# Kernel tuning notes

Hardware: AMD Instinct MI355X
Metric: run time of the kernel (lower is better)

## Reference

```python
import jax, jax.numpy as jnp
import numpy as np

B, D, H = 262144, 8, 64  # batch, in_out_dim, hidden_dim


def _lin_init(k, fan_in, fan_out):
    k1, k2 = jax.random.split(k)
    s = 1.0 / np.sqrt(fan_in)
    W = jax.random.uniform(k1, (fan_in, fan_out), minval=-s, maxval=s, dtype=jnp.float32)
    b = jax.random.uniform(k2, (fan_out,), minval=-s, maxval=s, dtype=jnp.float32)
    return W, b


def setup_inputs():
    key = jax.random.key(0)
    ks = jax.random.split(key, 12)
    w1_0, b1_0 = _lin_init(ks[0], D + 1, H)
    w1_1, b1_1 = _lin_init(ks[1], H, H)
    w1_2, b1_2 = _lin_init(ks[2], H, H)
    w1_o, b1_o = _lin_init(ks[3], H, D)
    w2_0, b2_0 = _lin_init(ks[4], D + 1, H)
    w2_1, b2_1 = _lin_init(ks[5], H, H)
    w2_2, b2_2 = _lin_init(ks[6], H, H)
    w2_o, b2_o = _lin_init(ks[7], H, 1)
    t = jax.random.uniform(ks[8], (), dtype=jnp.float32)
    z = jax.random.normal(ks[9], (B, D), dtype=jnp.float32)
    logp_z = jnp.zeros((B, 1), dtype=jnp.float32)
    return dict(t=t, z=z, logp_z=logp_z,
                w1_0=w1_0, b1_0=b1_0, w1_1=w1_1, b1_1=b1_1, w1_2=w1_2, b1_2=b1_2,
                w1_o=w1_o, b1_o=b1_o,
                w2_0=w2_0, b2_0=b2_0, w2_1=w2_1, b2_1=b2_1, w2_2=w2_2, b2_2=b2_2,
                w2_o=w2_o, b2_o=b2_o)


def reference(t, z, logp_z,
              w1_0, b1_0, w1_1, b1_1, w1_2, b1_2, w1_o, b1_o,
              w2_0, b2_0, w2_1, b2_1, w2_2, b2_2, w2_o, b2_o):
    Bz, Dz = z.shape
    tcol = jnp.full((Bz, 1), t, dtype=z.dtype)  # t repeated per-sample, detached constant

    def net1(zz):  # HyperNetwork1: dz/dt field, Tanh MLP, (B,D+1)->(B,D)
        s = jnp.concatenate([tcol, zz], axis=1)
        x = jnp.tanh(s @ w1_0 + b1_0)
        x = jnp.tanh(x @ w1_1 + b1_1)
        x = jnp.tanh(x @ w1_2 + b1_2)
        return x @ w1_o + b1_o

    dz_dt = net1(z)

    # HyperNetwork2: growth term g, (B,D+1)->(B,1)
    s = jnp.concatenate([tcol, z], axis=1)
    x = jnp.tanh(s @ w2_0 + b2_0)
    x = jnp.tanh(x @ w2_1 + b2_1)
    x = jnp.tanh(x @ w2_2 + b2_2)
    g = x @ w2_o + b2_o

    # Exact trace of d(dz_dt)/dz via D forward-mode JVPs (vectorized, replaces
    # the per-dim autograd.grad loop in trace_df_dz).
    eye = jnp.eye(Dz, dtype=z.dtype)
    jv = jax.vmap(lambda e: jax.jvp(net1, (z,), (jnp.broadcast_to(e, z.shape),))[1])(eye)  # (D,B,D)
    trace = jnp.diagonal(jv, axis1=0, axis2=2).sum(-1)  # (B,)

    dlogp_z_dt = g - trace[:, None]
    return (dz_dt, dlogp_z_dt, g)
```

## Files before the change

### kernel.cpp

```cpp
#include <hip/hip_runtime.h>


#define BATCH 262144

typedef _Float16 h16;
typedef __attribute__((ext_vector_type(8))) _Float16 half8;
typedef __attribute__((ext_vector_type(4))) float f32x4;

#define MFMA16(a, b, c) __builtin_amdgcn_mfma_f32_16x16x32_f16((a), (b), (c), 0, 0, 0)

#define WS_A   0
#define WS_WO  61440
#define WS_E   62464
#define WS_B   64512
#define WS_BO  66048

__device__ __forceinline__ float tanh_fast(float x) {
    float e = __builtin_amdgcn_exp2f(x * 2.8853900817779268f);
    return 1.0f - 2.0f * __builtin_amdgcn_rcpf(e + 1.0f);
}

__global__ void __launch_bounds__(256) prep(
    const float* __restrict__ w1_0, const float* __restrict__ w1_1,
    const float* __restrict__ w1_2, const float* __restrict__ w1_o,
    const float* __restrict__ w2_0, const float* __restrict__ w2_1,
    const float* __restrict__ w2_2, const float* __restrict__ w2_o,
    const float* __restrict__ b1_0, const float* __restrict__ b1_1,
    const float* __restrict__ b1_2, const float* __restrict__ b1_o,
    const float* __restrict__ b2_0, const float* __restrict__ b2_1,
    const float* __restrict__ b2_2, char* __restrict__ ws)
{
    int t = blockIdx.x * 256 + threadIdx.x;
    if (t < 3840) {
        int slot = t >> 6, lane = t & 63;
        int mrow = lane & 15, kg = lane >> 4;
        half8 v;
        #pragma unroll
        for (int kk = 0; kk < 8; ++kk) {
            int mt = 0, ks = 0;
            float val = 0.0f;
            if (slot < 4) {
                mt = slot; int k = kg * 8 + kk; int m = mt * 16 + mrow;
                val = (k < 9) ? w1_0[k * 64 + m] : 0.0f;
            } else if (slot < 12) {
                int s = slot - 4; mt = s >> 1; ks = s & 1;
                int k = ks * 32 + kg * 8 + kk; int m = mt * 16 + mrow;
                val = w1_1[k * 64 + m];
            } else if (slot < 20) {
                int s = slot - 12; mt = s >> 1; ks = s & 1;
                int k = ks * 32 + kg * 8 + kk; int m = mt * 16 + mrow;
                val = w1_2[k * 64 + m];
            } else if (slot < 22) {
                ks = slot - 20; int k = ks * 32 + kg * 8 + kk;
                val = (mrow < 8) ? w1_o[k * 8 + mrow] : 0.0f;
            } else if (slot < 26) {
                mt = slot - 22; int k = kg * 8 + kk; int m = mt * 16 + mrow;
                val = (k < 9) ? w2_0[k * 64 + m] : 0.0f;
            } else if (slot < 34) {
                int s = slot - 26; mt = s >> 1; ks = s & 1;
                int k = ks * 32 + kg * 8 + kk; int m = mt * 16 + mrow;
                val = w2_1[k * 64 + m];
            } else if (slot < 42) {
                int s = slot - 34; mt = s >> 1; ks = s & 1;
                int k = ks * 32 + kg * 8 + kk; int m = mt * 16 + mrow;
                val = w2_2[k * 64 + m];
            } else if (slot < 44) {
                ks = slot - 42; int k = ks * 32 + kg * 8 + kk;
                val = (mrow == 0) ? w2_o[k] : 0.0f;
            } else if (slot < 52) {
                int s = slot - 44; mt = s >> 1; ks = s & 1;
                int k = ks * 32 + kg * 8 + kk; int m = mt * 16 + mrow;
                val = w1_2[m * 64 + k];
            } else {
                int s = slot - 52; mt = s >> 1; ks = s & 1;
                int k = ks * 32 + kg * 8 + kk; int m = mt * 16 + mrow;
                val = w1_1[m * 64 + k];
            }
            v[kk] = (h16)val;
        }
        *(half8*)((h16*)(ws + WS_A) + (size_t)slot * 512 + (size_t)lane * 8) = v;
    } else if (t < 4352) {
        int e = t - 3840; int d = e >> 6, k = e & 63;
        ((h16*)(ws + WS_WO))[e] = (h16)w1_o[k * 8 + d];
    } else if (t < 4864) {
        int e = t - 4352; int d = e >> 6, g = (e >> 4) & 3, tr = e & 15;
        int mt = tr >> 2, r = tr & 3;
        int k = 16 * mt + 4 * g + r;
        ((float*)(ws + WS_E))[e] = w1_0[(d + 1) * 64 + k];
    } else if (t < 5248) {
        int e = t - 4864; int layer = e >> 6, i = e & 63;
        int g = i >> 4, mt = (i >> 2) & 3, r = i & 3;
        int m = 16 * mt + 4 * g + r;
        const float* bsrc = (layer == 0) ? b1_0 : (layer == 1) ? b1_1 :
                            (layer == 2) ? b1_2 : (layer == 3) ? b2_0 :
                            (layer == 4) ? b2_1 : b2_2;
        ((float*)(ws + WS_B))[e] = bsrc[m];
    } else if (t < 5264) {
        int i = t - 5248; int g = i >> 2, r = i & 3;
        int m = 4 * g + r;
        ((float*)(ws + WS_BO))[i] = (m < 8) ? b1_o[m] : 0.0f;
    }
}

__global__ void __launch_bounds__(256) cnf_mfma(
    const float* __restrict__ tp, const float* __restrict__ zp,
    const float* __restrict__ b2_o, const char* __restrict__ ws,
    float* __restrict__ out)
{
    __shared__ __align__(16) h16 xbuf[4][1024];
    __shared__ __align__(16) h16 t3buf[4][1024];

    const int lane = threadIdx.x & 63;
    const int wv = threadIdx.x >> 6;
    const int c = lane & 15;
    const int g = lane >> 4;
    const int sIdx = blockIdx.x * 64 + wv * 16 + c;
    const int swz = (c & 7) << 3;

    const h16*   wsA  = (const h16*)(ws + WS_A);
    const h16*   wsWo = (const h16*)(ws + WS_WO);
    const float* wsE  = (const float*)(ws + WS_E);
    const float* wsB  = (const float*)(ws + WS_B);
    const float* wsBo = (const float*)(ws + WS_BO);
    h16* xb  = xbuf[wv];
    h16* t3b = t3buf[wv];

    const float tt = tp[0];
    const f32x4 zl = *(const f32x4*)(zp + (size_t)sIdx * 8);
    const f32x4 zh = *(const f32x4*)(zp + (size_t)sIdx * 8 + 4);

    half8 b0f;
    #pragma unroll
    for (int i = 0; i < 8; ++i) b0f[i] = (h16)0.0f;
    if (g == 0) {
        b0f[0] = (h16)tt;
        b0f[1] = (h16)zl[0]; b0f[2] = (h16)zl[1]; b0f[3] = (h16)zl[2];
        b0f[4] = (h16)zl[3]; b0f[5] = (h16)zh[0]; b0f[6] = (h16)zh[1];
        b0f[7] = (h16)zh[2];
    } else if (g == 1) {
        b0f[0] = (h16)zh[3];
    }

    f32x4 d[4], t1v[4], t2v[4];

    #pragma unroll
    for (int mt = 0; mt < 4; ++mt) {
        f32x4 acc = *(const f32x4*)(wsB + 0 * 64 + g * 16 + mt * 4);
        d[mt] = MFMA16(*(const half8*)(wsA + (0 + mt) * 512 + lane * 8), b0f, acc);
    }
    #pragma unroll
    for (int mt = 0; mt < 4; ++mt) {
        union { h16 h[4]; uint2 u; } px;
        #pragma unroll
        for (int r = 0; r < 4; ++r) {
            float x = tanh_fast(d[mt][r]);
            t1v[mt][r] = fmaf(-x, x, 1.0f);
            px.h[r] = (h16)x;
        }
        *(uint2*)&xb[(c * 64 + mt * 16 + 4 * g) ^ swz] = px.u;
    }

    {
        half8 bf0 = *(const half8*)&xb[(c * 64 + 8 * g) ^ swz];
        half8 bf1 = *(const half8*)&xb[(c * 64 + 32 + 8 * g) ^ swz];
        #pragma unroll
        for (int mt = 0; mt < 4; ++mt) {
            f32x4 acc = *(const f32x4*)(wsB + 1 * 64 + g * 16 + mt * 4);
            acc = MFMA16(*(const half8*)(wsA + (4 + mt * 2) * 512 + lane * 8), bf0, acc);
            acc = MFMA16(*(const half8*)(wsA + (5 + mt * 2) * 512 + lane * 8), bf1, acc);
            d[mt] = acc;
        }
    }
    #pragma unroll
    for (int mt = 0; mt < 4; ++mt) {
        union { h16 h[4]; uint2 u; } px;
        #pragma unroll
        for (int r = 0; r < 4; ++r) {
            float x = tanh_fast(d[mt][r]);
            t2v[mt][r] = fmaf(-x, x, 1.0f);
            px.h[r] = (h16)x;
        }
        *(uint2*)&xb[(c * 64 + mt * 16 + 4 * g) ^ swz] = px.u;
    }

    {
        half8 bf0 = *(const half8*)&xb[(c * 64 + 8 * g) ^ swz];
        half8 bf1 = *(const half8*)&xb[(c * 64 + 32 + 8 * g) ^ swz];
        #pragma unroll
        for (int mt = 0; mt < 4; ++mt) {
            f32x4 acc = *(const f32x4*)(wsB + 2 * 64 + g * 16 + mt * 4);
            acc = MFMA16(*(const half8*)(wsA + (12 + mt * 2) * 512 + lane * 8), bf0, acc);
            acc = MFMA16(*(const half8*)(wsA + (13 + mt * 2) * 512 + lane * 8), bf1, acc);
            d[mt] = acc;
        }
    }
    #pragma unroll
    for (int mt = 0; mt < 4; ++mt) {
        union { h16 h[4]; uint2 u; } px, pt;
        #pragma unroll
        for (int r = 0; r < 4; ++r) {
            float x = tanh_fast(d[mt][r]);
            float tq = fmaf(-x, x, 1.0f);
            px.h[r] = (h16)x;
            pt.h[r] = (h16)tq;
        }
        int e = (c * 64 + mt * 16 + 4 * g) ^ swz;
        *(uint2*)&xb[e] = px.u;
        *(uint2*)&t3b[e] = pt.u;
    }

    {
        half8 bf0 = *(const half8*)&xb[(c * 64 + 8 * g) ^ swz];
        half8 bf1 = *(const half8*)&xb[(c * 64 + 32 + 8 * g) ^ swz];
        f32x4 dz = *(const f32x4*)(wsBo + g * 4);
        dz = MFMA16(*(const half8*)(wsA + 20 * 512 + lane * 8), bf0, dz);
        dz = MFMA16(*(const half8*)(wsA + 21 * 512 + lane * 8), bf1, dz);
        if (g < 2)
            *(f32x4*)(out + (size_t)sIdx * 8 + g * 4) = dz;
    }

    #pragma unroll
    for (int mt = 0; mt < 4; ++mt) {
        f32x4 acc = *(const f32x4*)(wsB + 3 * 64 + g * 16 + mt * 4);
        d[mt] = MFMA16(*(const half8*)(wsA + (22 + mt) * 512 + lane * 8), b0f, acc);
    }
    #pragma unroll
    for (int mt = 0; mt < 4; ++mt) {
        union { h16 h[4]; uint2 u; } px;
        #pragma unroll
        for (int r = 0; r < 4; ++r) px.h[r] = (h16)tanh_fast(d[mt][r]);
        *(uint2*)&xb[(c * 64 + mt * 16 + 4 * g) ^ swz] = px.u;
    }
    #pragma unroll 1
    for (int L = 0; L < 2; ++L) {
        int sbase = (L == 0) ? 26 : 34;
        half8 bf0 = *(const half8*)&xb[(c * 64 + 8 * g) ^ swz];
        half8 bf1 = *(const half8*)&xb[(c * 64 + 32 + 8 * g) ^ swz];
        #pragma unroll
        for (int mt = 0; mt < 4; ++mt) {
            f32x4 acc = *(const f32x4*)(wsB + (4 + L) * 64 + g * 16 + mt * 4);
            acc = MFMA16(*(const half8*)(wsA + (sbase + mt * 2) * 512 + lane * 8), bf0, acc);
            acc = MFMA16(*(const half8*)(wsA + (sbase + mt * 2 + 1) * 512 + lane * 8), bf1, acc);
            d[mt] = acc;
        }
        #pragma unroll
        for (int mt = 0; mt < 4; ++mt) {
            union { h16 h[4]; uint2 u; } px;
            #pragma unroll
            for (int r = 0; r < 4; ++r) px.h[r] = (h16)tanh_fast(d[mt][r]);
            *(uint2*)&xb[(c * 64 + mt * 16 + 4 * g) ^ swz] = px.u;
        }
    }
    float gval;
    {
        half8 bf0 = *(const half8*)&xb[(c * 64 + 8 * g) ^ swz];
        half8 bf1 = *(const half8*)&xb[(c * 64 + 32 + 8 * g) ^ swz];
        float b2 = b2_o[0];
        f32x4 acc = {b2, 0.0f, 0.0f, 0.0f};
        acc = MFMA16(*(const half8*)(wsA + 42 * 512 + lane * 8), bf0, acc);
        acc = MFMA16(*(const half8*)(wsA + 43 * 512 + lane * 8), bf1, acc);
        gval = acc[0];
    }

    float tr = 0.0f;
    #pragma unroll 1
    for (int d0 = 0; d0 < 8; ++d0) {
        f32x4 e0 = *(const f32x4*)(wsE + d0 * 64 + g * 16 + 0);
        f32x4 e1 = *(const f32x4*)(wsE + d0 * 64 + g * 16 + 4);
        f32x4 e2 = *(const f32x4*)(wsE + d0 * 64 + g * 16 + 8);
        f32x4 e3 = *(const f32x4*)(wsE + d0 * 64 + g * 16 + 12);
        half8 w0f = *(const half8*)(wsWo + d0 * 64 + 8 * g);
        half8 w1f = *(const half8*)(wsWo + d0 * 64 + 32 + 8 * g);
        half8 t3f0 = *(const half8*)&t3b[(c * 64 + 8 * g) ^ swz];
        half8 t3f1 = *(const half8*)&t3b[(c * 64 + 32 + 8 * g) ^ swz];
        half8 sA0 = t3f0 * w0f;
        half8 sA1 = t3f1 * w1f;
        f32x4 rr[4];
        #pragma unroll
        for (int mt = 0; mt < 4; ++mt) {
            f32x4 acc = {0.0f, 0.0f, 0.0f, 0.0f};
            acc = MFMA16(*(const half8*)(wsA + (44 + mt * 2) * 512 + lane * 8), sA0, acc);
            acc = MFMA16(*(const half8*)(wsA + (45 + mt * 2) * 512 + lane * 8), sA1, acc);
            rr[mt] = acc;
        }
        #pragma unroll
        for (int mt = 0; mt < 4; ++mt) {
            union { h16 h[4]; uint2 u; } px;
            #pragma unroll
            for (int r = 0; r < 4; ++r)
                px.h[r] = (h16)(t2v[mt][r] * rr[mt][r]);
            *(uint2*)&xb[(c * 64 + mt * 16 + 4 * g) ^ swz] = px.u;
        }
        half8 sb0 = *(const half8*)&xb[(c * 64 + 8 * g) ^ swz];
        half8 sb1 = *(const half8*)&xb[(c * 64 + 32 + 8 * g) ^ swz];
        #pragma unroll
        for (int mt = 0; mt < 4; ++mt) {
            f32x4 acc = {0.0f, 0.0f, 0.0f, 0.0f};
            acc = MFMA16(*(const half8*)(wsA + (52 + mt * 2) * 512 + lane * 8), sb0, acc);
            acc = MFMA16(*(const half8*)(wsA + (53 + mt * 2) * 512 + lane * 8), sb1, acc);
            d[mt] = acc;
        }
        #pragma unroll
        for (int r = 0; r < 4; ++r) {
            tr = fmaf(d[0][r] * t1v[0][r], e0[r], tr);
            tr = fmaf(d[1][r] * t1v[1][r], e1[r], tr);
            tr = fmaf(d[2][r] * t1v[2][r], e2[r], tr);
            tr = fmaf(d[3][r] * t1v[3][r], e3[r], tr);
        }
    }
    tr += __shfl_xor(tr, 16);
    tr += __shfl_xor(tr, 32);

    if (g == 0) {
        out[(size_t)BATCH * 8 + sIdx] = gval - tr;
        out[(size_t)BATCH * 9 + sIdx] = gval;
    }
}

extern "C" void kernel_launch(void* const* d_in, const int* in_sizes, int n_in,
                              void* d_out, int out_size, void* d_ws, size_t ws_size,
                              hipStream_t stream) {
    const float* tp   = (const float*)d_in[0];
    const float* zp   = (const float*)d_in[1];
    const float* w1_0 = (const float*)d_in[3];
    const float* b1_0 = (const float*)d_in[4];
    const float* w1_1 = (const float*)d_in[5];
    const float* b1_1 = (const float*)d_in[6];
    const float* w1_2 = (const float*)d_in[7];
    const float* b1_2 = (const float*)d_in[8];
    const float* w1_o = (const float*)d_in[9];
    const float* b1_o = (const float*)d_in[10];
    const float* w2_0 = (const float*)d_in[11];
    const float* b2_0 = (const float*)d_in[12];
    const float* w2_1 = (const float*)d_in[13];
    const float* b2_1 = (const float*)d_in[14];
    const float* w2_2 = (const float*)d_in[15];
    const float* b2_2 = (const float*)d_in[16];
    const float* w2_o = (const float*)d_in[17];
    const float* b2_o = (const float*)d_in[18];

    char* ws = (char*)d_ws;
    float* out = (float*)d_out;

    hipLaunchKernelGGL(prep, dim3(21), dim3(256), 0, stream,
                       w1_0, w1_1, w1_2, w1_o, w2_0, w2_1, w2_2, w2_o,
                       b1_0, b1_1, b1_2, b1_o, b2_0, b2_1, b2_2, ws);
    hipLaunchKernelGGL(cnf_mfma, dim3(BATCH / 64), dim3(256), 0, stream,
                       tp, zp, b2_o, ws, out);
}
```

Before: 186.3 us.

## Reorder trace loop before net2, drop t3 LDS buffer, pack fp16 conversions

```diff
diff --git a/kernel.cpp b/kernel.cpp
--- a/kernel.cpp
+++ b/kernel.cpp
@@ -4,6 +4,7 @@
 #define BATCH 262144
 
 typedef _Float16 h16;
+typedef __attribute__((ext_vector_type(2))) __fp16 f16x2;
 typedef __attribute__((ext_vector_type(8))) _Float16 half8;
 typedef __attribute__((ext_vector_type(4))) float f32x4;
 
@@ -108,7 +109,6 @@
     float* __restrict__ out)
 {
     __shared__ __align__(16) h16 xbuf[4][1024];
-    __shared__ __align__(16) h16 t3buf[4][1024];
 
     const int lane = threadIdx.x & 63;
     const int wv = threadIdx.x >> 6;
@@ -116,14 +116,19 @@
     const int g = lane >> 4;
     const int sIdx = blockIdx.x * 64 + wv * 16 + c;
     const int swz = (c & 7) << 3;
+    h16* xb = xbuf[wv];
+
+    int wadr[4];
+    #pragma unroll
+    for (int mt = 0; mt < 4; ++mt) wadr[mt] = (c * 64 + mt * 16 + 4 * g) ^ swz;
+    const int radr0 = (c * 64 + 8 * g) ^ swz;
+    const int radr1 = (c * 64 + 32 + 8 * g) ^ swz;
 
     const h16*   wsA  = (const h16*)(ws + WS_A);
     const h16*   wsWo = (const h16*)(ws + WS_WO);
     const float* wsE  = (const float*)(ws + WS_E);
     const float* wsB  = (const float*)(ws + WS_B);
     const float* wsBo = (const float*)(ws + WS_BO);
-    h16* xb  = xbuf[wv];
-    h16* t3b = t3buf[wv];
 
     const float tt = tp[0];
     const f32x4 zl = *(const f32x4*)(zp + (size_t)sIdx * 8);
@@ -141,7 +146,8 @@
         b0f[0] = (h16)zh[3];
     }
 
-    f32x4 d[4], t1v[4], t2v[4];
+    f32x4 d[4], t1v[4];
+    f16x2 t2h[8];
 
     #pragma unroll
     for (int mt = 0; mt < 4; ++mt) {
@@ -150,19 +156,19 @@
     }
     #pragma unroll
     for (int mt = 0; mt < 4; ++mt) {
-        union { h16 h[4]; uint2 u; } px;
-        #pragma unroll
-        for (int r = 0; r < 4; ++r) {
-            float x = tanh_fast(d[mt][r]);
-            t1v[mt][r] = fmaf(-x, x, 1.0f);
-            px.h[r] = (h16)x;
-        }
-        *(uint2*)&xb[(c * 64 + mt * 16 + 4 * g) ^ swz] = px.u;
-    }
-
-    {
-        half8 bf0 = *(const half8*)&xb[(c * 64 + 8 * g) ^ swz];
-        half8 bf1 = *(const half8*)&xb[(c * 64 + 32 + 8 * g) ^ swz];
+        float x0 = tanh_fast(d[mt][0]), x1 = tanh_fast(d[mt][1]);
+        float x2 = tanh_fast(d[mt][2]), x3 = tanh_fast(d[mt][3]);
+        t1v[mt][0] = fmaf(-x0, x0, 1.0f); t1v[mt][1] = fmaf(-x1, x1, 1.0f);
+        t1v[mt][2] = fmaf(-x2, x2, 1.0f); t1v[mt][3] = fmaf(-x3, x3, 1.0f);
+        union { f16x2 h[2]; uint2 u; } pk;
+        pk.h[0] = __builtin_amdgcn_cvt_pkrtz(x0, x1);
+        pk.h[1] = __builtin_amdgcn_cvt_pkrtz(x2, x3);
+        *(uint2*)&xb[wadr[mt]] = pk.u;
+    }
+
+    {
+        half8 bf0 = *(const half8*)&xb[radr0];
+        half8 bf1 = *(const half8*)&xb[radr1];
         #pragma unroll
         for (int mt = 0; mt < 4; ++mt) {
             f32x4 acc = *(const f32x4*)(wsB + 1 * 64 + g * 16 + mt * 4);
@@ -173,19 +179,19 @@
     }
     #pragma unroll
     for (int mt = 0; mt < 4; ++mt) {
-        union { h16 h[4]; uint2 u; } px;
-        #pragma unroll
-        for (int r = 0; r < 4; ++r) {
-            float x = tanh_fast(d[mt][r]);
-            t2v[mt][r] = fmaf(-x, x, 1.0f);
-            px.h[r] = (h16)x;
-        }
-        *(uint2*)&xb[(c * 64 + mt * 16 + 4 * g) ^ swz] = px.u;
-    }
-
-    {
-        half8 bf0 = *(const half8*)&xb[(c * 64 + 8 * g) ^ swz];
-        half8 bf1 = *(const half8*)&xb[(c * 64 + 32 + 8 * g) ^ swz];
+        float x0 = tanh_fast(d[mt][0]), x1 = tanh_fast(d[mt][1]);
+        float x2 = tanh_fast(d[mt][2]), x3 = tanh_fast(d[mt][3]);
+        t2h[2 * mt]     = __builtin_amdgcn_cvt_pkrtz(fmaf(-x0, x0, 1.0f), fmaf(-x1, x1, 1.0f));
+        t2h[2 * mt + 1] = __builtin_amdgcn_cvt_pkrtz(fmaf(-x2, x2, 1.0f), fmaf(-x3, x3, 1.0f));
+        union { f16x2 h[2]; uint2 u; } pk;
+        pk.h[0] = __builtin_amdgcn_cvt_pkrtz(x0, x1);
+        pk.h[1] = __builtin_amdgcn_cvt_pkrtz(x2, x3);
+        *(uint2*)&xb[wadr[mt]] = pk.u;
+    }
+
+    {
+        half8 bf0 = *(const half8*)&xb[radr0];
+        half8 bf1 = *(const half8*)&xb[radr1];
         #pragma unroll
         for (int mt = 0; mt < 4; ++mt) {
             f32x4 acc = *(const f32x4*)(wsB + 2 * 64 + g * 16 + mt * 4);
@@ -196,29 +202,86 @@
     }
     #pragma unroll
     for (int mt = 0; mt < 4; ++mt) {
-        union { h16 h[4]; uint2 u; } px, pt;
-        #pragma unroll
-        for (int r = 0; r < 4; ++r) {
-            float x = tanh_fast(d[mt][r]);
-            float tq = fmaf(-x, x, 1.0f);
-            px.h[r] = (h16)x;
-            pt.h[r] = (h16)tq;
-        }
-        int e = (c * 64 + mt * 16 + 4 * g) ^ swz;
-        *(uint2*)&xb[e] = px.u;
-        *(uint2*)&t3b[e] = pt.u;
-    }
-
-    {
-        half8 bf0 = *(const half8*)&xb[(c * 64 + 8 * g) ^ swz];
-        half8 bf1 = *(const half8*)&xb[(c * 64 + 32 + 8 * g) ^ swz];
+        float x0 = tanh_fast(d[mt][0]), x1 = tanh_fast(d[mt][1]);
+        float x2 = tanh_fast(d[mt][2]), x3 = tanh_fast(d[mt][3]);
+        union { f16x2 h[2]; uint2 u; } pk;
+        pk.h[0] = __builtin_amdgcn_cvt_pkrtz(x0, x1);
+        pk.h[1] = __builtin_amdgcn_cvt_pkrtz(x2, x3);
+        *(uint2*)&xb[wadr[mt]] = pk.u;
+    }
+
+    half8 gA[8];
+    #pragma unroll
+    for (int s = 0; s < 8; ++s)
+        gA[s] = *(const half8*)(wsA + (44 + s) * 512 + lane * 8);
+
+    half8 xf0 = *(const half8*)&xb[radr0];
+    half8 xf1 = *(const half8*)&xb[radr1];
+
+    {
         f32x4 dz = *(const f32x4*)(wsBo + g * 4);
-        dz = MFMA16(*(const half8*)(wsA + 20 * 512 + lane * 8), bf0, dz);
-        dz = MFMA16(*(const half8*)(wsA + 21 * 512 + lane * 8), bf1, dz);
+        dz = MFMA16(*(const half8*)(wsA + 20 * 512 + lane * 8), xf0, dz);
+        dz = MFMA16(*(const half8*)(wsA + 21 * 512 + lane * 8), xf1, dz);
         if (g < 2)
             *(f32x4*)(out + (size_t)sIdx * 8 + g * 4) = dz;
     }
 
+    half8 one8;
+    #pragma unroll
+    for (int i = 0; i < 8; ++i) one8[i] = (h16)1.0f;
+    const half8 t3f0 = one8 - xf0 * xf0;
+    const half8 t3f1 = one8 - xf1 * xf1;
+
+    f32x4 tacc[4];
+    #pragma unroll
+    for (int mt = 0; mt < 4; ++mt) tacc[mt] = (f32x4){0.0f, 0.0f, 0.0f, 0.0f};
+
+    #pragma unroll 1
+    for (int d0 = 0; d0 < 8; ++d0) {
+        half8 w0f = *(const half8*)(wsWo + d0 * 64 + 8 * g);
+        half8 w1f = *(const half8*)(wsWo + d0 * 64 + 32 + 8 * g);
+        half8 sA0 = t3f0 * w0f;
+        half8 sA1 = t3f1 * w1f;
+        f32x4 rr[4];
+        #pragma unroll
+        for (int mt = 0; mt < 4; ++mt) {
+            f32x4 acc = {0.0f, 0.0f, 0.0f, 0.0f};
+            acc = MFMA16(gA[2 * mt], sA0, acc);
+            acc = MFMA16(gA[2 * mt + 1], sA1, acc);
+            rr[mt] = acc;
+        }
+        #pragma unroll
+        for (int mt = 0; mt < 4; ++mt) {
+            union { f16x2 h[2]; uint2 u; } pk;
+            pk.h[0] = __builtin_amdgcn_cvt_pkrtz(rr[mt][0], rr[mt][1]) * t2h[2 * mt];
+            pk.h[1] = __builtin_amdgcn_cvt_pkrtz(rr[mt][2], rr[mt][3]) * t2h[2 * mt + 1];
+            *(uint2*)&xb[wadr[mt]] = pk.u;
+        }
+        half8 sb0 = *(const half8*)&xb[radr0];
+        half8 sb1 = *(const half8*)&xb[radr1];
+        #pragma unroll
+        for (int mt = 0; mt < 4; ++mt) {
+            f32x4 acc = {0.0f, 0.0f, 0.0f, 0.0f};
+            acc = MFMA16(*(const half8*)(wsA + (52 + mt * 2) * 512 + lane * 8), sb0, acc);
+            acc = MFMA16(*(const half8*)(wsA + (53 + mt * 2) * 512 + lane * 8), sb1, acc);
+            f32x4 e = *(const f32x4*)(wsE + d0 * 64 + g * 16 + mt * 4);
+            #pragma unroll
+            for (int r = 0; r < 4; ++r) tacc[mt][r] = fmaf(acc[r], e[r], tacc[mt][r]);
+        }
+    }
+    float tr;
+    {
+        f32x4 tm = tacc[0] * t1v[0];
+        #pragma unroll
+        for (int mt = 1; mt < 4; ++mt) {
+            #pragma unroll
+            for (int r = 0; r < 4; ++r) tm[r] = fmaf(tacc[mt][r], t1v[mt][r], tm[r]);
+        }
+        tr = tm[0] + tm[1] + tm[2] + tm[3];
+    }
+    tr += __shfl_xor(tr, 16);
+    tr += __shfl_xor(tr, 32);
+
     #pragma unroll
     for (int mt = 0; mt < 4; ++mt) {
         f32x4 acc = *(const f32x4*)(wsB + 3 * 64 + g * 16 + mt * 4);
@@ -226,16 +289,16 @@
     }
     #pragma unroll
     for (int mt = 0; mt < 4; ++mt) {
-        union { h16 h[4]; uint2 u; } px;
-        #pragma unroll
-        for (int r = 0; r < 4; ++r) px.h[r] = (h16)tanh_fast(d[mt][r]);
-        *(uint2*)&xb[(c * 64 + mt * 16 + 4 * g) ^ swz] = px.u;
+        union { f16x2 h[2]; uint2 u; } pk;
+        pk.h[0] = __builtin_amdgcn_cvt_pkrtz(tanh_fast(d[mt][0]), tanh_fast(d[mt][1]));
+        pk.h[1] = __builtin_amdgcn_cvt_pkrtz(tanh_fast(d[mt][2]), tanh_fast(d[mt][3]));
+        *(uint2*)&xb[wadr[mt]] = pk.u;
     }
     #pragma unroll 1
     for (int L = 0; L < 2; ++L) {
         int sbase = (L == 0) ? 26 : 34;
-        half8 bf0 = *(const half8*)&xb[(c * 64 + 8 * g) ^ swz];
-        half8 bf1 = *(const half8*)&xb[(c * 64 + 32 + 8 * g) ^ swz];
+        half8 bf0 = *(const half8*)&xb[radr0];
+        half8 bf1 = *(const half8*)&xb[radr1];
         #pragma unroll
         for (int mt = 0; mt < 4; ++mt) {
             f32x4 acc = *(const f32x4*)(wsB + (4 + L) * 64 + g * 16 + mt * 4);
@@ -245,71 +308,21 @@
         }
         #pragma unroll
         for (int mt = 0; mt < 4; ++mt) {
-            union { h16 h[4]; uint2 u; } px;
-            #pragma unroll
-            for (int r = 0; r < 4; ++r) px.h[r] = (h16)tanh_fast(d[mt][r]);
-            *(uint2*)&xb[(c * 64 + mt * 16 + 4 * g) ^ swz] = px.u;
+            union { f16x2 h[2]; uint2 u; } pk;
+            pk.h[0] = __builtin_amdgcn_cvt_pkrtz(tanh_fast(d[mt][0]), tanh_fast(d[mt][1]));
+            pk.h[1] = __builtin_amdgcn_cvt_pkrtz(tanh_fast(d[mt][2]), tanh_fast(d[mt][3]));
+            *(uint2*)&xb[wadr[mt]] = pk.u;
         }
     }
     float gval;
     {
-        half8 bf0 = *(const half8*)&xb[(c * 64 + 8 * g) ^ swz];
-        half8 bf1 = *(const half8*)&xb[(c * 64 + 32 + 8 * g) ^ swz];
-        float b2 = b2_o[0];
-        f32x4 acc = {b2, 0.0f, 0.0f, 0.0f};
+        half8 bf0 = *(const half8*)&xb[radr0];
+        half8 bf1 = *(const half8*)&xb[radr1];
+        f32x4 acc = {b2_o[0], 0.0f, 0.0f, 0.0f};
         acc = MFMA16(*(const half8*)(wsA + 42 * 512 + lane * 8), bf0, acc);
         acc = MFMA16(*(const half8*)(wsA + 43 * 512 + lane * 8), bf1, acc);
         gval = acc[0];
     }
-
-    float tr = 0.0f;
-    #pragma unroll 1
-    for (int d0 = 0; d0 < 8; ++d0) {
-        f32x4 e0 = *(const f32x4*)(wsE + d0 * 64 + g * 16 + 0);
-        f32x4 e1 = *(const f32x4*)(wsE + d0 * 64 + g * 16 + 4);
-        f32x4 e2 = *(const f32x4*)(wsE + d0 * 64 + g * 16 + 8);
-        f32x4 e3 = *(const f32x4*)(wsE + d0 * 64 + g * 16 + 12);
-        half8 w0f = *(const half8*)(wsWo + d0 * 64 + 8 * g);
-        half8 w1f = *(const half8*)(wsWo + d0 * 64 + 32 + 8 * g);
-        half8 t3f0 = *(const half8*)&t3b[(c * 64 + 8 * g) ^ swz];
-        half8 t3f1 = *(const half8*)&t3b[(c * 64 + 32 + 8 * g) ^ swz];
-        half8 sA0 = t3f0 * w0f;
-        half8 sA1 = t3f1 * w1f;
-        f32x4 rr[4];
-        #pragma unroll
-        for (int mt = 0; mt < 4; ++mt) {
-            f32x4 acc = {0.0f, 0.0f, 0.0f, 0.0f};
-            acc = MFMA16(*(const half8*)(wsA + (44 + mt * 2) * 512 + lane * 8), sA0, acc);
-            acc = MFMA16(*(const half8*)(wsA + (45 + mt * 2) * 512 + lane * 8), sA1, acc);
-            rr[mt] = acc;
-        }
-        #pragma unroll
-        for (int mt = 0; mt < 4; ++mt) {
-            union { h16 h[4]; uint2 u; } px;
-            #pragma unroll
-            for (int r = 0; r < 4; ++r)
-                px.h[r] = (h16)(t2v[mt][r] * rr[mt][r]);
-            *(uint2*)&xb[(c * 64 + mt * 16 + 4 * g) ^ swz] = px.u;
-        }
-        half8 sb0 = *(const half8*)&xb[(c * 64 + 8 * g) ^ swz];
-        half8 sb1 = *(const half8*)&xb[(c * 64 + 32 + 8 * g) ^ swz];
-        #pragma unroll
-        for (int mt = 0; mt < 4; ++mt) {
-            f32x4 acc = {0.0f, 0.0f, 0.0f, 0.0f};
-            acc = MFMA16(*(const half8*)(wsA + (52 + mt * 2) * 512 + lane * 8), sb0, acc);
-            acc = MFMA16(*(const half8*)(wsA + (53 + mt * 2) * 512 + lane * 8), sb1, acc);
-            d[mt] = acc;
-        }
-        #pragma unroll
-        for (int r = 0; r < 4; ++r) {
-            tr = fmaf(d[0][r] * t1v[0][r], e0[r], tr);
-            tr = fmaf(d[1][r] * t1v[1][r], e1[r], tr);
-            tr = fmaf(d[2][r] * t1v[2][r], e2[r], tr);
-            tr = fmaf(d[3][r] * t1v[3][r], e3[r], tr);
-        }
-    }
-    tr += __shfl_xor(tr, 16);
-    tr += __shfl_xor(tr, 32);
 
     if (g == 0) {
         out[(size_t)BATCH * 8 + sIdx] = gval - tr;
```

Result: slower. 194.8 us (+4.5%).
